# Performance work log

Hardware: AMD Instinct MI355X
Metric: run time of the kernel (lower is better)

Reference implementation:

```python
import jax, jax.numpy as jnp
import numpy as np

B, S, D, H = 2, 4096, 512, 8
HD = D // H

def setup_inputs() -> dict:
    key = jax.random.key(0)
    ks = jax.random.split(key, 11)
    s = 1.0 / np.sqrt(D)
    return {
        "x": jax.random.normal(ks[0], (B, S, D), jnp.float32),
        "y": jax.random.normal(ks[1], (B, S, D), jnp.float32),
        "z": jax.random.normal(ks[2], (B, S, D), jnp.float32),
        "Wq": jax.random.normal(ks[3], (D, D), jnp.float32) * s,
        "bq": jnp.zeros((D,), jnp.float32),
        "Wk": jax.random.normal(ks[4], (D, D), jnp.float32) * s,
        "bk": jnp.zeros((D,), jnp.float32),
        "Wv": jax.random.normal(ks[5], (D, D), jnp.float32) * s,
        "bv": jnp.zeros((D,), jnp.float32),
        "Wp": jax.random.normal(ks[6], (D, D), jnp.float32) * s,
        "bp": jnp.zeros((D,), jnp.float32),
    }

def reference(x, y, z, Wq, bq, Wk, bk, Wv, bv, Wp, bp):
    # q/k/v projections, split heads: [B,S,D] -> [B,H,S,HD]
    def heads(t):
        return t.reshape(B, -1, H, HD).transpose(0, 2, 1, 3)
    q = heads(x @ Wq + bq)
    k = heads(y @ Wk + bk)
    v = heads(z @ Wv + bv)
    att = jnp.einsum('bhqd,bhkd->bhqk', q, k) / np.sqrt(HD).astype(np.float32)
    att = jax.nn.softmax(att, axis=-1)  # dropout is identity in eval mode
    out = jnp.einsum('bhqk,bhkd->bhqd', att, v)
    out = out.transpose(0, 2, 1, 3).reshape(B, -1, D)
    return out @ Wp + bp
```

## Files before the change

### kernel.cpp

```cpp
#include <hip/hip_runtime.h>
#include <math.h>

#define B_ 2
#define S_ 4096
#define D_ 512
#define H_ 8
#define HD_ 64
#define NROW_ (B_ * S_)
#define NELEM_ ((size_t)NROW_ * D_)
#define WELEM_ ((size_t)D_ * D_)

typedef _Float16 half8 __attribute__((ext_vector_type(8)));
typedef _Float16 half4v __attribute__((ext_vector_type(4)));
typedef _Float16 half2v __attribute__((ext_vector_type(2)));
typedef __fp16 fp16x2 __attribute__((ext_vector_type(2)));
typedef float floatx4 __attribute__((ext_vector_type(4)));

__device__ __forceinline__ half8 cvt_half8(float4 a, float4 b) {
  fp16x2 l0 = __builtin_amdgcn_cvt_pkrtz(a.x, a.y);
  fp16x2 l1 = __builtin_amdgcn_cvt_pkrtz(a.z, a.w);
  fp16x2 l2 = __builtin_amdgcn_cvt_pkrtz(b.x, b.y);
  fp16x2 l3 = __builtin_amdgcn_cvt_pkrtz(b.z, b.w);
  half8 h;
  h[0] = l0[0]; h[1] = l0[1]; h[2] = l1[0]; h[3] = l1[1];
  h[4] = l2[0]; h[5] = l2[1]; h[6] = l3[0]; h[7] = l3[1];
  return h;
}

struct WPtrs { const float *W0, *W1, *W2, *W3; };

__global__ void wT4_kernel(WPtrs p, _Float16* __restrict__ WTbase) {
  __shared__ float tl[32][33];
  const int z = blockIdx.z;
  const float* W = z == 0 ? p.W0 : z == 1 ? p.W1 : z == 2 ? p.W2 : p.W3;
  const float scale = z == 0 ? 0.125f : 1.0f;
  _Float16* Wt = WTbase + (size_t)z * WELEM_;
  const int t = threadIdx.x;
  const int k0 = blockIdx.y * 32, n0 = blockIdx.x * 32;
  const int r = t >> 3, c0 = (t & 7) * 4;
  const float4 v = *(const float4*)&W[(size_t)(k0 + r) * D_ + n0 + c0];
  tl[r][c0 + 0] = v.x; tl[r][c0 + 1] = v.y;
  tl[r][c0 + 2] = v.z; tl[r][c0 + 3] = v.w;
  __syncthreads();
  half4v hv;
#pragma unroll
  for (int j = 0; j < 4; ++j) hv[j] = (_Float16)(tl[c0 + j][r] * scale);
  *(half4v*)&Wt[(size_t)(n0 + r) * D_ + k0 + c0] = hv;
}

__global__ void vT_kernel(const _Float16* __restrict__ Vh,
                          _Float16* __restrict__ VhT) {
  __shared__ alignas(16) _Float16 T[64][72];
  const int t = threadIdx.x;
  const int s0 = blockIdx.x * 64;
  const int h = blockIdx.y, b = blockIdx.z;
  const int srow = t >> 3, soff = (t & 7) * 8;
#pragma unroll
  for (int i = 0; i < 2; ++i)
    *(half8*)&T[srow + 32 * i][soff] = *(const half8*)
        &Vh[(size_t)(b * S_ + s0 + srow + 32 * i) * D_ + h * HD_ + soff];
  __syncthreads();
  const size_t obase = (size_t)(b * H_ + h) * HD_ * S_;
#pragma unroll
  for (int i = 0; i < 2; ++i) {
    half8 o;
#pragma unroll
    for (int j = 0; j < 8; ++j) {
      const int ka = soff + j;
      const int key = 16 * (ka & 3) + (ka >> 2);
      o[j] = T[key][srow + 32 * i];
    }
    *(half8*)&VhT[obase + (size_t)(srow + 32 * i) * S_ + s0 + soff] = o;
  }
}

template <bool AF16, bool OUT16, int BM>
__device__ __forceinline__ void gemm_body(
    const void* __restrict__ Av, const _Float16* __restrict__ Bt,
    const float* __restrict__ bias, void* __restrict__ Cout, float bscale,
    int bx, int by, int tid) {
  constexpr int MT = BM / 32;
  __shared__ alignas(16) _Float16 As[BM][72];
  __shared__ alignas(16) _Float16 Bs[128][72];

  const int w = tid >> 6, lane = tid & 63;
  const int m = lane & 15, quad = lane >> 4;
  const int row0 = by * BM, col0 = bx * 128;
  const int wr = (w >> 1) * (BM / 2), wc = (w & 1) * 64;
  const int srow = tid >> 3, soff = (tid & 7) * 8;

  const _Float16* A16 = (const _Float16*)Av;
  const float* A32 = (const float*)Av;

  floatx4 acc[MT][4];
#pragma unroll
  for (int i = 0; i < MT; ++i)
#pragma unroll
    for (int j = 0; j < 4; ++j) acc[i][j] = floatx4{0.f, 0.f, 0.f, 0.f};

  half8 pa16[MT];
  float4 pa32[MT][2];
  half8 pb[4];
#pragma unroll
  for (int i = 0; i < MT; ++i) {
    const size_t ar = (size_t)(row0 + srow + 32 * i) * D_ + soff;
    if (AF16) pa16[i] = *(const half8*)&A16[ar];
    else { pa32[i][0] = *(const float4*)&A32[ar];
           pa32[i][1] = *(const float4*)&A32[ar + 4]; }
  }
#pragma unroll
  for (int i = 0; i < 4; ++i)
    pb[i] = *(const half8*)&Bt[(size_t)(col0 + srow + 32 * i) * D_ + soff];

  for (int kt = 0; kt < D_ / 64; ++kt) {
    if (kt) __syncthreads();
#pragma unroll
    for (int i = 0; i < MT; ++i)
      *(half8*)&As[srow + 32 * i][soff] =
          AF16 ? pa16[i] : cvt_half8(pa32[i][0], pa32[i][1]);
#pragma unroll
    for (int i = 0; i < 4; ++i) *(half8*)&Bs[srow + 32 * i][soff] = pb[i];
    __syncthreads();
    if (kt < D_ / 64 - 1) {
      const int kc = (kt + 1) * 64 + soff;
#pragma unroll
      for (int i = 0; i < MT; ++i) {
        const size_t ar = (size_t)(row0 + srow + 32 * i) * D_ + kc;
        if (AF16) pa16[i] = *(const half8*)&A16[ar];
        else { pa32[i][0] = *(const float4*)&A32[ar];
               pa32[i][1] = *(const float4*)&A32[ar + 4]; }
      }
#pragma unroll
      for (int i = 0; i < 4; ++i)
        pb[i] = *(const half8*)&Bt[(size_t)(col0 + srow + 32 * i) * D_ + kc];
    }
#pragma unroll
    for (int h = 0; h < 2; ++h) {
      half8 af[MT], bf[4];
#pragma unroll
      for (int mt = 0; mt < MT; ++mt)
        af[mt] = *(const half8*)&As[wr + mt * 16 + m][h * 32 + quad * 8];
#pragma unroll
      for (int nt = 0; nt < 4; ++nt)
        bf[nt] = *(const half8*)&Bs[wc + nt * 16 + m][h * 32 + quad * 8];
#pragma unroll
      for (int mt = 0; mt < MT; ++mt)
#pragma unroll
        for (int nt = 0; nt < 4; ++nt)
          acc[mt][nt] = __builtin_amdgcn_mfma_f32_16x16x32_f16(
              af[mt], bf[nt], acc[mt][nt], 0, 0, 0);
    }
  }

  float bv[4];
#pragma unroll
  for (int nt = 0; nt < 4; ++nt)
    bv[nt] = bias[col0 + wc + nt * 16 + m] * bscale;
#pragma unroll
  for (int mt = 0; mt < MT; ++mt)
#pragma unroll
    for (int nt = 0; nt < 4; ++nt)
#pragma unroll
      for (int r = 0; r < 4; ++r) {
        const int row = row0 + wr + mt * 16 + quad * 4 + r;
        const int col = col0 + wc + nt * 16 + m;
        const float vout = acc[mt][nt][r] + bv[nt];
        if (OUT16)
          ((_Float16*)Cout)[(size_t)row * D_ + col] = (_Float16)vout;
        else
          ((float*)Cout)[(size_t)row * D_ + col] = vout;
      }
}

struct QkvPtrs { const float *A0, *A1, *A2, *b0, *b1, *b2; };

__global__ __launch_bounds__(256, 3) void qkv_gemm_kernel(
    QkvPtrs p, const _Float16* __restrict__ WT, _Float16* __restrict__ Cb) {
  const int z = blockIdx.z;
  const float* A = z == 0 ? p.A0 : z == 1 ? p.A1 : p.A2;
  const float* bias = z == 0 ? p.b0 : z == 1 ? p.b1 : p.b2;
  gemm_body<false, true, 128>(A, WT + (size_t)z * WELEM_, bias,
                              Cb + (size_t)z * NELEM_, z == 0 ? 0.125f : 1.0f,
                              blockIdx.x, blockIdx.y, threadIdx.x);
}

__global__ __launch_bounds__(256, 2) void out_gemm_kernel(
    const _Float16* __restrict__ Oh, const _Float16* __restrict__ WpT,
    const float* __restrict__ bp, float* __restrict__ out) {
  gemm_body<true, false, 64>(Oh, WpT, bp, out, 1.0f, blockIdx.x, blockIdx.y,
                             threadIdx.x);
}

__global__ __launch_bounds__(256, 2) void attn_mfma_kernel(
    const _Float16* __restrict__ Qg, const _Float16* __restrict__ Kg,
    const _Float16* __restrict__ VT, _Float16* __restrict__ Og) {
  __shared__ alignas(16) _Float16 Ks[64][72];
  __shared__ alignas(16) _Float16 Vt[64][72];
  __shared__ alignas(16) _Float16 Ps[128][72];

  const int t = threadIdx.x;
  const int w = t >> 6;
  const int lane = t & 63;
  const int m = lane & 15;
  const int quad = lane >> 4;
  const int q0 = blockIdx.x * 128;
  const size_t base =
      (size_t)blockIdx.z * ((size_t)S_ * D_) + (size_t)blockIdx.y * HD_;
  const size_t vbase = (size_t)(blockIdx.z * H_ + blockIdx.y) * HD_ * S_;

  half8 qf[2][2];
#pragma unroll
  for (int s = 0; s < 2; ++s)
#pragma unroll
    for (int h = 0; h < 2; ++h)
      qf[s][h] = *(const half8*)&Qg[base +
          (size_t)(q0 + s * 64 + w * 16 + m) * D_ + h * 32 + quad * 8];

  floatx4 oacc[2][4];
  float lpart[2][4];
#pragma unroll
  for (int s = 0; s < 2; ++s)
#pragma unroll
    for (int n = 0; n < 4; ++n) oacc[s][n] = floatx4{0.f, 0.f, 0.f, 0.f};
#pragma unroll
  for (int s = 0; s < 2; ++s)
#pragma unroll
    for (int r = 0; r < 4; ++r) lpart[s][r] = 0.f;

  const int srow = t >> 3, soff = (t & 7) * 8;

  half8 pk[2], pv[2];
#pragma unroll
  for (int i = 0; i < 2; ++i) {
    pk[i] = *(const half8*)&Kg[base + (size_t)(srow + 32 * i) * D_ + soff];
    pv[i] = *(const half8*)&VT[vbase + (size_t)(srow + 32 * i) * S_ + soff];
  }

  for (int kt = 0; kt < S_ / 64; ++kt) {
    if (kt) __syncthreads();
#pragma unroll
    for (int i = 0; i < 2; ++i) {
      *(half8*)&Ks[srow + 32 * i][soff] = pk[i];
      *(half8*)&Vt[srow + 32 * i][soff] = pv[i];
    }
    __syncthreads();

    if (kt < S_ / 64 - 1) {
      const int k1 = (kt + 1) * 64;
#pragma unroll
      for (int i = 0; i < 2; ++i) {
        pk[i] = *(const half8*)
            &Kg[base + (size_t)(k1 + srow + 32 * i) * D_ + soff];
        pv[i] = *(const half8*)
            &VT[vbase + (size_t)(srow + 32 * i) * S_ + k1 + soff];
      }
    }

    floatx4 sacc[2][4];
#pragma unroll
    for (int s = 0; s < 2; ++s)
#pragma unroll
      for (int n = 0; n < 4; ++n) sacc[s][n] = floatx4{0.f, 0.f, 0.f, 0.f};
#pragma unroll
    for (int n = 0; n < 4; ++n)
#pragma unroll
      for (int h = 0; h < 2; ++h) {
        const half8 bf = *(const half8*)&Ks[n * 16 + m][h * 32 + quad * 8];
        sacc[0][n] = __builtin_amdgcn_mfma_f32_16x16x32_f16(
            qf[0][h], bf, sacc[0][n], 0, 0, 0);
        sacc[1][n] = __builtin_amdgcn_mfma_f32_16x16x32_f16(
            qf[1][h], bf, sacc[1][n], 0, 0, 0);
      }

#pragma unroll
    for (int s = 0; s < 2; ++s) {
      const int prow = s * 64 + w * 16 + quad * 4;
#pragma unroll
      for (int r = 0; r < 4; ++r) {
        const float p0 = __expf(fminf(sacc[s][0][r], 11.f));
        const float p1 = __expf(fminf(sacc[s][1][r], 11.f));
        const float p2 = __expf(fminf(sacc[s][2][r], 11.f));
        const float p3 = __expf(fminf(sacc[s][3][r], 11.f));
        lpart[s][r] += (p0 + p1) + (p2 + p3);
        const fp16x2 plo = __builtin_amdgcn_cvt_pkrtz(p0, p1);
        const fp16x2 phi = __builtin_amdgcn_cvt_pkrtz(p2, p3);
        half4v ph;
        ph[0] = plo[0]; ph[1] = plo[1]; ph[2] = phi[0]; ph[3] = phi[1];
        *(half4v*)&Ps[prow + r][4 * m] = ph;
      }
    }

    half8 af[2][2];
#pragma unroll
    for (int s = 0; s < 2; ++s) {
      af[s][0] = *(const half8*)&Ps[s * 64 + w * 16 + m][quad * 8];
      af[s][1] = *(const half8*)&Ps[s * 64 + w * 16 + m][32 + quad * 8];
    }
#pragma unroll
    for (int n = 0; n < 4; ++n) {
      const half8 b0 = *(const half8*)&Vt[n * 16 + m][quad * 8];
      const half8 b1 = *(const half8*)&Vt[n * 16 + m][32 + quad * 8];
#pragma unroll
      for (int s = 0; s < 2; ++s) {
        oacc[s][n] = __builtin_amdgcn_mfma_f32_16x16x32_f16(
            af[s][0], b0, oacc[s][n], 0, 0, 0);
        oacc[s][n] = __builtin_amdgcn_mfma_f32_16x16x32_f16(
            af[s][1], b1, oacc[s][n], 0, 0, 0);
      }
    }
  }

  float linv[2][4];
#pragma unroll
  for (int s = 0; s < 2; ++s)
#pragma unroll
    for (int r = 0; r < 4; ++r) {
      float ls = lpart[s][r];
      ls += __shfl_xor(ls, 1);
      ls += __shfl_xor(ls, 2);
      ls += __shfl_xor(ls, 4);
      ls += __shfl_xor(ls, 8);
      linv[s][r] = 1.0f / ls;
    }
#pragma unroll
  for (int s = 0; s < 2; ++s)
#pragma unroll
    for (int n = 0; n < 4; ++n)
#pragma unroll
      for (int r = 0; r < 4; ++r)
        Og[base + (size_t)(q0 + s * 64 + w * 16 + quad * 4 + r) * D_ +
           n * 16 + m] = (_Float16)(oacc[s][n][r] * linv[s][r]);
}

extern "C" void kernel_launch(void* const* d_in, const int* in_sizes, int n_in,
                              void* d_out, int out_size, void* d_ws,
                              size_t ws_size, hipStream_t stream) {
  const float* x  = (const float*)d_in[0];
  const float* y  = (const float*)d_in[1];
  const float* z  = (const float*)d_in[2];
  const float* Wq = (const float*)d_in[3];
  const float* bq = (const float*)d_in[4];
  const float* Wk = (const float*)d_in[5];
  const float* bk = (const float*)d_in[6];
  const float* Wv = (const float*)d_in[7];
  const float* bv = (const float*)d_in[8];
  const float* Wp = (const float*)d_in[9];
  const float* bp = (const float*)d_in[10];

  _Float16* hws = (_Float16*)d_ws;
  _Float16* WT  = hws;
  _Float16* Qh  = WT + 4 * WELEM_;
  _Float16* Kh  = Qh + NELEM_;
  _Float16* Vh  = Kh + NELEM_;
  _Float16* Oh  = Vh + NELEM_;
  _Float16* VhT = Oh + NELEM_;

  WPtrs wp{Wq, Wk, Wv, Wp};
  wT4_kernel<<<dim3(16, 16, 4), 256, 0, stream>>>(wp, WT);

  QkvPtrs qp{x, y, z, bq, bk, bv};
  qkv_gemm_kernel<<<dim3(4, 64, 3), 256, 0, stream>>>(qp, WT, Qh);

  vT_kernel<<<dim3(S_ / 64, H_, B_), 256, 0, stream>>>(Vh, VhT);

  attn_mfma_kernel<<<dim3(S_ / 128, H_, B_), 256, 0, stream>>>(Qh, Kh, VhT, Oh);

  out_gemm_kernel<<<dim3(4, 128), 256, 0, stream>>>(Oh, WT + 3 * WELEM_, bp,
                                                    (float*)d_out);
}
```

Baseline: 259.1 us.

## Double-buffer K/V tiles in LDS and split attention work across 8 waves

```diff
diff --git a/kernel.cpp b/kernel.cpp
--- a/kernel.cpp
+++ b/kernel.cpp
@@ -191,11 +191,11 @@
                              threadIdx.x);
 }
 
-__global__ __launch_bounds__(256, 2) void attn_mfma_kernel(
+__global__ __launch_bounds__(512, 4) void attn_mfma_kernel(
     const _Float16* __restrict__ Qg, const _Float16* __restrict__ Kg,
     const _Float16* __restrict__ VT, _Float16* __restrict__ Og) {
-  __shared__ alignas(16) _Float16 Ks[64][72];
-  __shared__ alignas(16) _Float16 Vt[64][72];
+  __shared__ alignas(16) _Float16 Ks[2][64][72];
+  __shared__ alignas(16) _Float16 Vt[2][64][72];
   __shared__ alignas(16) _Float16 Ps[128][72];
 
   const int t = threadIdx.x;
@@ -208,128 +208,106 @@
       (size_t)blockIdx.z * ((size_t)S_ * D_) + (size_t)blockIdx.y * HD_;
   const size_t vbase = (size_t)(blockIdx.z * H_ + blockIdx.y) * HD_ * S_;
 
-  half8 qf[2][2];
-#pragma unroll
-  for (int s = 0; s < 2; ++s)
-#pragma unroll
-    for (int h = 0; h < 2; ++h)
-      qf[s][h] = *(const half8*)&Qg[base +
-          (size_t)(q0 + s * 64 + w * 16 + m) * D_ + h * 32 + quad * 8];
-
-  floatx4 oacc[2][4];
-  float lpart[2][4];
-#pragma unroll
-  for (int s = 0; s < 2; ++s)
-#pragma unroll
-    for (int n = 0; n < 4; ++n) oacc[s][n] = floatx4{0.f, 0.f, 0.f, 0.f};
-#pragma unroll
-  for (int s = 0; s < 2; ++s)
-#pragma unroll
-    for (int r = 0; r < 4; ++r) lpart[s][r] = 0.f;
-
-  const int srow = t >> 3, soff = (t & 7) * 8;
-
-  half8 pk[2], pv[2];
-#pragma unroll
-  for (int i = 0; i < 2; ++i) {
-    pk[i] = *(const half8*)&Kg[base + (size_t)(srow + 32 * i) * D_ + soff];
-    pv[i] = *(const half8*)&VT[vbase + (size_t)(srow + 32 * i) * S_ + soff];
-  }
-
-  for (int kt = 0; kt < S_ / 64; ++kt) {
-    if (kt) __syncthreads();
-#pragma unroll
-    for (int i = 0; i < 2; ++i) {
-      *(half8*)&Ks[srow + 32 * i][soff] = pk[i];
-      *(half8*)&Vt[srow + 32 * i][soff] = pv[i];
-    }
+  half8 qf[2];
+#pragma unroll
+  for (int h = 0; h < 2; ++h)
+    qf[h] = *(const half8*)
+        &Qg[base + (size_t)(q0 + w * 16 + m) * D_ + h * 32 + quad * 8];
+
+  floatx4 oacc[4];
+  float lpart[4];
+#pragma unroll
+  for (int n = 0; n < 4; ++n) oacc[n] = floatx4{0.f, 0.f, 0.f, 0.f};
+#pragma unroll
+  for (int r = 0; r < 4; ++r) lpart[r] = 0.f;
+
+  const int srow = t >> 3;
+  const int soff = (t & 7) * 8;
+
+  half8 pk = *(const half8*)&Kg[base + (size_t)srow * D_ + soff];
+  half8 pv = *(const half8*)&VT[vbase + (size_t)srow * S_ + soff];
+  *(half8*)&Ks[0][srow][soff] = pk;
+  *(half8*)&Vt[0][srow][soff] = pv;
+  pk = *(const half8*)&Kg[base + (size_t)(64 + srow) * D_ + soff];
+  pv = *(const half8*)&VT[vbase + (size_t)srow * S_ + 64 + soff];
+  __syncthreads();
+
+  constexpr int NT = S_ / 64;
+  for (int kt = 0; kt < NT; ++kt) {
+    const int cur = kt & 1;
+    if (kt + 1 < NT) {
+      *(half8*)&Ks[cur ^ 1][srow][soff] = pk;
+      *(half8*)&Vt[cur ^ 1][srow][soff] = pv;
+      if (kt + 2 < NT) {
+        const int k2 = (kt + 2) * 64;
+        pk = *(const half8*)&Kg[base + (size_t)(k2 + srow) * D_ + soff];
+        pv = *(const half8*)&VT[vbase + (size_t)srow * S_ + k2 + soff];
+      }
+    }
+
+    floatx4 sacc[4];
+#pragma unroll
+    for (int n = 0; n < 4; ++n) sacc[n] = floatx4{0.f, 0.f, 0.f, 0.f};
+    __builtin_amdgcn_s_setprio(1);
+#pragma unroll
+    for (int n = 0; n < 4; ++n)
+#pragma unroll
+      for (int h = 0; h < 2; ++h) {
+        const half8 bf =
+            *(const half8*)&Ks[cur][n * 16 + m][h * 32 + quad * 8];
+        sacc[n] = __builtin_amdgcn_mfma_f32_16x16x32_f16(
+            qf[h], bf, sacc[n], 0, 0, 0);
+      }
+    __builtin_amdgcn_s_setprio(0);
+
+    const int prow = w * 16 + quad * 4;
+#pragma unroll
+    for (int r = 0; r < 4; ++r) {
+      const float p0 = __expf(fminf(sacc[0][r], 11.f));
+      const float p1 = __expf(fminf(sacc[1][r], 11.f));
+      const float p2 = __expf(fminf(sacc[2][r], 11.f));
+      const float p3 = __expf(fminf(sacc[3][r], 11.f));
+      lpart[r] += (p0 + p1) + (p2 + p3);
+      const fp16x2 plo = __builtin_amdgcn_cvt_pkrtz(p0, p1);
+      const fp16x2 phi = __builtin_amdgcn_cvt_pkrtz(p2, p3);
+      half4v ph;
+      ph[0] = plo[0]; ph[1] = plo[1]; ph[2] = phi[0]; ph[3] = phi[1];
+      *(half4v*)&Ps[prow + r][4 * m] = ph;
+    }
+
+    const half8 af0 = *(const half8*)&Ps[w * 16 + m][quad * 8];
+    const half8 af1 = *(const half8*)&Ps[w * 16 + m][32 + quad * 8];
+    __builtin_amdgcn_s_setprio(1);
+#pragma unroll
+    for (int n = 0; n < 4; ++n) {
+      const half8 b0 = *(const half8*)&Vt[cur][n * 16 + m][quad * 8];
+      const half8 b1 = *(const half8*)&Vt[cur][n * 16 + m][32 + quad * 8];
+      oacc[n] = __builtin_amdgcn_mfma_f32_16x16x32_f16(
+          af0, b0, oacc[n], 0, 0, 0);
+      oacc[n] = __builtin_amdgcn_mfma_f32_16x16x32_f16(
+          af1, b1, oacc[n], 0, 0, 0);
+    }
+    __builtin_amdgcn_s_setprio(0);
+
     __syncthreads();
-
-    if (kt < S_ / 64 - 1) {
-      const int k1 = (kt + 1) * 64;
-#pragma unroll
-      for (int i = 0; i < 2; ++i) {
-        pk[i] = *(const half8*)
-            &Kg[base + (size_t)(k1 + srow + 32 * i) * D_ + soff];
-        pv[i] = *(const half8*)
-            &VT[vbase + (size_t)(srow + 32 * i) * S_ + k1 + soff];
-      }
-    }
-
-    floatx4 sacc[2][4];
-#pragma unroll
-    for (int s = 0; s < 2; ++s)
-#pragma unroll
-      for (int n = 0; n < 4; ++n) sacc[s][n] = floatx4{0.f, 0.f, 0.f, 0.f};
-#pragma unroll
-    for (int n = 0; n < 4; ++n)
-#pragma unroll
-      for (int h = 0; h < 2; ++h) {
-        const half8 bf = *(const half8*)&Ks[n * 16 + m][h * 32 + quad * 8];
-        sacc[0][n] = __builtin_amdgcn_mfma_f32_16x16x32_f16(
-            qf[0][h], bf, sacc[0][n], 0, 0, 0);
-        sacc[1][n] = __builtin_amdgcn_mfma_f32_16x16x32_f16(
-            qf[1][h], bf, sacc[1][n], 0, 0, 0);
-      }
-
-#pragma unroll
-    for (int s = 0; s < 2; ++s) {
-      const int prow = s * 64 + w * 16 + quad * 4;
-#pragma unroll
-      for (int r = 0; r < 4; ++r) {
-        const float p0 = __expf(fminf(sacc[s][0][r], 11.f));
-        const float p1 = __expf(fminf(sacc[s][1][r], 11.f));
-        const float p2 = __expf(fminf(sacc[s][2][r], 11.f));
-        const float p3 = __expf(fminf(sacc[s][3][r], 11.f));
-        lpart[s][r] += (p0 + p1) + (p2 + p3);
-        const fp16x2 plo = __builtin_amdgcn_cvt_pkrtz(p0, p1);
-        const fp16x2 phi = __builtin_amdgcn_cvt_pkrtz(p2, p3);
-        half4v ph;
-        ph[0] = plo[0]; ph[1] = plo[1]; ph[2] = phi[0]; ph[3] = phi[1];
-        *(half4v*)&Ps[prow + r][4 * m] = ph;
-      }
-    }
-
-    half8 af[2][2];
-#pragma unroll
-    for (int s = 0; s < 2; ++s) {
-      af[s][0] = *(const half8*)&Ps[s * 64 + w * 16 + m][quad * 8];
-      af[s][1] = *(const half8*)&Ps[s * 64 + w * 16 + m][32 + quad * 8];
-    }
-#pragma unroll
-    for (int n = 0; n < 4; ++n) {
-      const half8 b0 = *(const half8*)&Vt[n * 16 + m][quad * 8];
-      const half8 b1 = *(const half8*)&Vt[n * 16 + m][32 + quad * 8];
-#pragma unroll
-      for (int s = 0; s < 2; ++s) {
-        oacc[s][n] = __builtin_amdgcn_mfma_f32_16x16x32_f16(
-            af[s][0], b0, oacc[s][n], 0, 0, 0);
-        oacc[s][n] = __builtin_amdgcn_mfma_f32_16x16x32_f16(
-            af[s][1], b1, oacc[s][n], 0, 0, 0);
-      }
-    }
-  }
-
-  float linv[2][4];
-#pragma unroll
-  for (int s = 0; s < 2; ++s)
-#pragma unroll
-    for (int r = 0; r < 4; ++r) {
-      float ls = lpart[s][r];
-      ls += __shfl_xor(ls, 1);
-      ls += __shfl_xor(ls, 2);
-      ls += __shfl_xor(ls, 4);
-      ls += __shfl_xor(ls, 8);
-      linv[s][r] = 1.0f / ls;
-    }
-#pragma unroll
-  for (int s = 0; s < 2; ++s)
-#pragma unroll
-    for (int n = 0; n < 4; ++n)
-#pragma unroll
-      for (int r = 0; r < 4; ++r)
-        Og[base + (size_t)(q0 + s * 64 + w * 16 + quad * 4 + r) * D_ +
-           n * 16 + m] = (_Float16)(oacc[s][n][r] * linv[s][r]);
+  }
+
+  float linv[4];
+#pragma unroll
+  for (int r = 0; r < 4; ++r) {
+    float ls = lpart[r];
+    ls += __shfl_xor(ls, 1);
+    ls += __shfl_xor(ls, 2);
+    ls += __shfl_xor(ls, 4);
+    ls += __shfl_xor(ls, 8);
+    linv[r] = 1.0f / ls;
+  }
+#pragma unroll
+  for (int n = 0; n < 4; ++n)
+#pragma unroll
+    for (int r = 0; r < 4; ++r)
+      Og[base + (size_t)(q0 + w * 16 + quad * 4 + r) * D_ + n * 16 + m] =
+          (_Float16)(oacc[n][r] * linv[r]);
 }
 
 extern "C" void kernel_launch(void* const* d_in, const int* in_sizes, int n_in,
@@ -363,7 +341,7 @@
 
   vT_kernel<<<dim3(S_ / 64, H_, B_), 256, 0, stream>>>(Vh, VhT);
 
-  attn_mfma_kernel<<<dim3(S_ / 128, H_, B_), 256, 0, stream>>>(Qh, Kh, VhT, Oh);
+  attn_mfma_kernel<<<dim3(S_ / 128, H_, B_), 512, 0, stream>>>(Qh, Kh, VhT, Oh);
 
   out_gemm_kernel<<<dim3(4, 128), 256, 0, stream>>>(Oh, WT + 3 * WELEM_, bp,
                                                     (float*)d_out);
```

After: 258.7 us. About the same (-0.2%).
